# Kernel tuning notes

Measured on AMD Instinct MI355X. Metric: run time of the kernel, lower is better.

## Reference

```python
import jax, jax.numpy as jnp
import numpy as np

N = 100_000   # nodes
E = 1_600_000 # edges per edge type
DIN = 128     # input_dim
DH = 128      # prot_hidden_dim
L = 3         # prot_num_layers
EPS = 1e-5


def setup_inputs() -> dict:
    key = jax.random.key(0)
    ks = jax.random.split(key, 8)
    s = 1.0 / np.sqrt(DH)
    return {
        "x": jax.random.normal(ks[0], (N, DIN), jnp.float32),
        "src": jax.random.randint(ks[1], (3, E), 0, N, jnp.int32),
        "dst": jax.random.randint(ks[2], (3, E), 0, N, jnp.int32),
        "gc_W0": jax.random.normal(ks[3], (3, DIN, DH), jnp.float32) * s,
        "gc_b0": jnp.zeros((3, DH), jnp.float32),
        "gc_W": jax.random.normal(ks[4], (L - 1, 3, DH, DH), jnp.float32) * s,
        "gc_b": jnp.zeros((L - 1, 3, DH), jnp.float32),
        "fc_W": jax.random.normal(ks[5], (L, DH, DH), jnp.float32) * s,
        "fc_b": jnp.zeros((L, DH), jnp.float32),
        "bn_gamma": jnp.ones((L, DH), jnp.float32),
        "bn_beta": jnp.zeros((L, DH), jnp.float32),
    }


def _graph_conv(x, src, dst, W, b):
    # DGL GraphConv, norm='both': D_in^{-1/2} A D_out^{-1/2} X W + b
    ones = jnp.ones(src.shape[0], x.dtype)
    deg_out = jnp.clip(jax.ops.segment_sum(ones, src, num_segments=N), 1.0)
    deg_in = jnp.clip(jax.ops.segment_sum(ones, dst, num_segments=N), 1.0)
    # apply weight first (same math; keeps gathered message width = DH)
    h = (x * jax.lax.rsqrt(deg_out)[:, None]) @ W  # [N, DH]
    agg = jax.ops.segment_sum(h[src], dst, num_segments=N)  # gather + scatter-add
    return agg * jax.lax.rsqrt(deg_in)[:, None] + b


def _batchnorm(x, gamma, beta):
    # training-mode BatchNorm1d: biased batch statistics
    mu = jnp.mean(x, axis=0)
    var = jnp.mean(jnp.square(x - mu), axis=0)
    return (x - mu) * jax.lax.rsqrt(var + EPS) * gamma + beta


def reference(x, src, dst, gc_W0, gc_b0, gc_W, gc_b, fc_W, fc_b, bn_gamma, bn_beta):
    h = x
    for l in range(L):
        W = gc_W0 if l == 0 else gc_W[l - 1]
        b = gc_b0 if l == 0 else gc_b[l - 1]
        # HeteroGraphConv with aggregate='sum' over 3 edge types
        out = _graph_conv(h, src[0], dst[0], W[0], b[0])
        for e in range(1, 3):
            out = out + _graph_conv(h, src[e], dst[e], W[e], b[e])
        # FC -> ReLU -> BatchNorm (dropout = identity in eval mode)
        h = _batchnorm(jax.nn.relu(out @ fc_W[l] + fc_b[l]), bn_gamma[l], bn_beta[l])
    return h
```

## Files before the change

kernel.cpp:

```cpp
#include <hip/hip_runtime.h>


#define EPSV 1e-5f
#define CH 8192
#define MAXNB 512

typedef __attribute__((ext_vector_type(8))) short s8v;
typedef __attribute__((ext_vector_type(4))) float f4v;

__global__ void coarse_hist(const int* __restrict__ src, const int* __restrict__ dst,
                            int* __restrict__ chd, int* __restrict__ chs,
                            int E, int NB) {
    __shared__ int hd[MAXNB], hs[MAXNB];
    int t = blockIdx.y;
    for (int i = threadIdx.x; i < NB; i += 256) { hd[i] = 0; hs[i] = 0; }
    __syncthreads();
    int base = blockIdx.x * CH;
    int end = base + CH < E ? base + CH : E;
    const int* sp = src + (size_t)t * E;
    const int* dp = dst + (size_t)t * E;
    for (int i = base + threadIdx.x; i < end; i += 256) {
        atomicAdd(&hd[dp[i] >> 8], 1);
        atomicAdd(&hs[sp[i] >> 8], 1);
    }
    __syncthreads();
    for (int b = threadIdx.x; b < NB; b += 256) {
        if (hd[b]) atomicAdd(&chd[t * NB + b], hd[b]);
        if (hs[b]) atomicAdd(&chs[t * NB + b], hs[b]);
    }
}

__global__ void scan_off(const int* __restrict__ chd, const int* __restrict__ chs,
                         int* __restrict__ offd, int* __restrict__ offs,
                         int* __restrict__ gcd, int* __restrict__ gcs,
                         int* __restrict__ rowptr, int NB, int N, int E) {
    __shared__ int s[MAXNB];
    int tid = threadIdx.x;
    for (int a = 0; a < 6; ++a) {
        const int* h = (a < 3) ? chd + a * NB : chs + (a - 3) * NB;
        int* off = (a < 3) ? offd + a * (NB + 1) : offs + (a - 3) * (NB + 1);
        int* gc = (a < 3) ? gcd + a * NB : gcs + (a - 3) * NB;
        s[tid] = (tid < NB) ? h[tid] : 0;
        __syncthreads();
        for (int o = 1; o < MAXNB; o <<= 1) {
            int v = (tid >= o) ? s[tid - o] : 0;
            __syncthreads();
            s[tid] += v;
            __syncthreads();
        }
        if (tid < NB) {
            off[tid + 1] = s[tid];
            if (tid == 0) off[0] = 0;
        }
        __syncthreads();
        if (tid < NB) gc[tid] = off[tid];
        __syncthreads();
    }
    if (tid < 3) rowptr[tid * (N + 1) + N] = E;
}

__global__ void scatter_coarse(const int* __restrict__ src, const int* __restrict__ dst,
                               int* __restrict__ gcd, int* __restrict__ gcs,
                               int* __restrict__ dbuf, unsigned char* __restrict__ sbuf,
                               int E, int NB) {
    __shared__ int hd[MAXNB], hs[MAXNB], bd[MAXNB], bs[MAXNB];
    int t = blockIdx.y;
    for (int i = threadIdx.x; i < NB; i += 256) { hd[i] = 0; hs[i] = 0; }
    __syncthreads();
    int base = blockIdx.x * CH;
    int end = base + CH < E ? base + CH : E;
    const int* sp = src + (size_t)t * E;
    const int* dp = dst + (size_t)t * E;
    for (int i = base + threadIdx.x; i < end; i += 256) {
        atomicAdd(&hd[dp[i] >> 8], 1);
        atomicAdd(&hs[sp[i] >> 8], 1);
    }
    __syncthreads();
    for (int b = threadIdx.x; b < NB; b += 256) {
        bd[b] = hd[b] ? atomicAdd(&gcd[t * NB + b], hd[b]) : 0;
        bs[b] = hs[b] ? atomicAdd(&gcs[t * NB + b], hs[b]) : 0;
        hd[b] = 0;
        hs[b] = 0;
    }
    __syncthreads();
    for (int i = base + threadIdx.x; i < end; i += 256) {
        int sv = sp[i], dv = dp[i];
        int pb = dv >> 8;
        int pos = bd[pb] + atomicAdd(&hd[pb], 1);
        dbuf[(size_t)t * E + pos] = (sv << 8) | (dv & 255);
        int sb = sv >> 8;
        int ps = bs[sb] + atomicAdd(&hs[sb], 1);
        sbuf[(size_t)t * E + ps] = (unsigned char)(sv & 255);
    }
}

__global__ void fine_dst(const int* __restrict__ dbuf, const int* __restrict__ offd,
                         int* __restrict__ esrc, int* __restrict__ rowptr,
                         float* __restrict__ dri, int E, int N, int NB) {
    __shared__ int h[256], sc[256], cur[256];
    int b = blockIdx.x, t = blockIdx.y;
    int tid = threadIdx.x;
    h[tid] = 0;
    __syncthreads();
    int beg = offd[t * (NB + 1) + b], end = offd[t * (NB + 1) + b + 1];
    const int* dp = dbuf + (size_t)t * E;
    for (int i = beg + tid; i < end; i += 256) atomicAdd(&h[dp[i] & 255], 1);
    __syncthreads();
    sc[tid] = h[tid];
    __syncthreads();
    for (int o = 1; o < 256; o <<= 1) {
        int v = (tid >= o) ? sc[tid - o] : 0;
        __syncthreads();
        sc[tid] += v;
        __syncthreads();
    }
    int excl = sc[tid] - h[tid];
    cur[tid] = excl;
    int node = b * 256 + tid;
    if (node < N) {
        rowptr[t * (N + 1) + node] = beg + excl;
        int dg = h[tid] < 1 ? 1 : h[tid];
        dri[(size_t)t * N + node] = rsqrtf((float)dg);
    }
    __syncthreads();
    for (int i = beg + tid; i < end; i += 256) {
        int v = dp[i];
        int f = v & 255;
        int pos = beg + atomicAdd(&cur[f], 1);
        esrc[(size_t)t * E + pos] = v >> 8;
    }
}

__global__ void fine_src(const unsigned char* __restrict__ sbuf, const int* __restrict__ offs,
                         float* __restrict__ dro, int E, int N, int NB) {
    __shared__ int h[256];
    int b = blockIdx.x, t = blockIdx.y;
    int tid = threadIdx.x;
    h[tid] = 0;
    __syncthreads();
    int beg = offs[t * (NB + 1) + b], end = offs[t * (NB + 1) + b + 1];
    const unsigned char* sp = sbuf + (size_t)t * E;
    for (int i = beg + tid; i < end; i += 256) atomicAdd(&h[sp[i]], 1);
    __syncthreads();
    int node = b * 256 + tid;
    if (node < N) {
        int dg = h[tid] < 1 ? 1 : h[tid];
        dro[(size_t)t * N + node] = rsqrtf((float)dg);
    }
}

__device__ __forceinline__ unsigned int bfr(float f) {
    unsigned int u = __float_as_uint(f);
    return (u + 0x7FFFu + ((u >> 16) & 1u)) >> 16;
}
__device__ __forceinline__ unsigned int pack2(float lo, float hi) {
    return bfr(lo) | (bfr(hi) << 16);
}
__device__ __forceinline__ float blo(unsigned int u) { return __uint_as_float(u << 16); }
__device__ __forceinline__ float bhi(unsigned int u) { return __uint_as_float(u & 0xFFFF0000u); }

__global__ void cvt_bf16(const float* __restrict__ h, unsigned short* __restrict__ h2,
                         int total8) {
    int i = blockIdx.x * 256 + threadIdx.x;
    if (i >= total8) return;
    const float4* hp = (const float4*)h + (size_t)i * 2;
    float4 v0 = hp[0], v1 = hp[1];
    uint4 o;
    o.x = pack2(v0.x, v0.y);
    o.y = pack2(v0.z, v0.w);
    o.z = pack2(v1.x, v1.y);
    o.w = pack2(v1.z, v1.w);
    ((uint4*)h2)[i] = o;
}

__global__ void pack_w(const float* __restrict__ gcW0, const float* __restrict__ gcW,
                       const float* __restrict__ fcW, unsigned short* __restrict__ Wg,
                       unsigned short* __restrict__ Wf) {
    int mat = blockIdx.x;
    const float* srcp;
    unsigned short* dstp;
    if (mat < 9) {
        int l = mat / 3, e = mat % 3;
        srcp = (l == 0) ? gcW0 + (size_t)e * 16384
                        : gcW + ((size_t)(l - 1) * 3 + e) * 16384;
        dstp = Wg + (size_t)mat * 16384;
    } else {
        srcp = fcW + (size_t)(mat - 9) * 16384;
        dstp = Wf + (size_t)(mat - 9) * 16384;
    }
    for (int p = threadIdx.x; p < 16384; p += 256) {
        int j = p & 7;
        int ln = (p >> 3) & 63;
        int nt = (p >> 9) & 7;
        int ks = p >> 12;
        int k = ks * 32 + (ln >> 4) * 8 + j;
        int n = nt * 16 + (ln & 15);
        dstp[p] = (unsigned short)bfr(srcp[k * 128 + n]);
    }
}

__launch_bounds__(256)
__global__ void agg_kernel(const unsigned short* __restrict__ h2, const int* __restrict__ rowptr,
                           const int* __restrict__ esrc, const float* __restrict__ dro,
                           const float* __restrict__ dri, unsigned short* __restrict__ z, int N) {
    int idx = blockIdx.x * 256 + threadIdx.x;
    int node = idx >> 5;
    int l2 = idx & 31;
    if (node >= N) return;
    int beg = rowptr[node];
    int end = rowptr[node + 1];
    const uint2* hp = (const uint2*)h2 + l2;
    float4 acc = make_float4(0.f, 0.f, 0.f, 0.f);
    int j = beg;
    for (; j + 4 <= end; j += 4) {
        int s0 = esrc[j], s1 = esrc[j + 1], s2 = esrc[j + 2], s3 = esrc[j + 3];
        float w0 = dro[s0], w1 = dro[s1], w2 = dro[s2], w3 = dro[s3];
        uint2 u0 = hp[(size_t)s0 * 32];
        uint2 u1 = hp[(size_t)s1 * 32];
        uint2 u2 = hp[(size_t)s2 * 32];
        uint2 u3 = hp[(size_t)s3 * 32];
        acc.x += w0 * blo(u0.x) + w1 * blo(u1.x) + w2 * blo(u2.x) + w3 * blo(u3.x);
        acc.y += w0 * bhi(u0.x) + w1 * bhi(u1.x) + w2 * bhi(u2.x) + w3 * bhi(u3.x);
        acc.z += w0 * blo(u0.y) + w1 * blo(u1.y) + w2 * blo(u2.y) + w3 * blo(u3.y);
        acc.w += w0 * bhi(u0.y) + w1 * bhi(u1.y) + w2 * bhi(u2.y) + w3 * bhi(u3.y);
    }
    for (; j < end; ++j) {
        int s0 = esrc[j];
        float w0 = dro[s0];
        uint2 u0 = hp[(size_t)s0 * 32];
        acc.x += w0 * blo(u0.x);
        acc.y += w0 * bhi(u0.x);
        acc.z += w0 * blo(u0.y);
        acc.w += w0 * bhi(u0.y);
    }
    float scl = dri[node];
    uint2 o;
    o.x = pack2(acc.x * scl, acc.y * scl);
    o.y = pack2(acc.z * scl, acc.w * scl);
    *(uint2*)(z + (size_t)node * 128 + l2 * 4) = o;
}

__launch_bounds__(256)
__global__ void mfma_gc(const unsigned short* __restrict__ z0,
                        const unsigned short* __restrict__ z1,
                        const unsigned short* __restrict__ z2,
                        const unsigned short* __restrict__ Wp,
                        const float* __restrict__ b3,
                        unsigned short* __restrict__ C, int M) {
    const int tid = threadIdx.x;
    const int l = tid & 63;
    const int wv = tid >> 6;
    const int wm = wv >> 1, wn = wv & 1;
    const int m0 = blockIdx.x * 128;
    const int lr = l & 15;
    const int lk = (l >> 4) * 8;
    f4v acc[4][4];
#pragma unroll
    for (int i = 0; i < 4; ++i)
#pragma unroll
        for (int j = 0; j < 4; ++j) acc[i][j] = (f4v){0.f, 0.f, 0.f, 0.f};

    int rowb[4];
#pragma unroll
    for (int mt = 0; mt < 4; ++mt) {
        int r = m0 + wm * 64 + mt * 16 + lr;
        rowb[mt] = (r < M) ? r : (M - 1);
    }
#pragma unroll
    for (int e = 0; e < 3; ++e) {
        const unsigned short* zp = (e == 0) ? z0 : (e == 1) ? z1 : z2;
        const unsigned short* wp = Wp + (size_t)e * 16384;
#pragma unroll
        for (int ks = 0; ks < 4; ++ks) {
            s8v a[4], b[4];
#pragma unroll
            for (int mt = 0; mt < 4; ++mt)
                a[mt] = *(const s8v*)(zp + (size_t)rowb[mt] * 128 + ks * 32 + lk);
#pragma unroll
            for (int nt = 0; nt < 4; ++nt)
                b[nt] = *(const s8v*)(wp + ks * 4096 + (wn * 4 + nt) * 512 + l * 8);
#pragma unroll
            for (int mt = 0; mt < 4; ++mt)
#pragma unroll
                for (int nt = 0; nt < 4; ++nt)
                    acc[mt][nt] = __builtin_amdgcn_mfma_f32_16x16x32_bf16(
                        a[mt], b[nt], acc[mt][nt], 0, 0, 0);
        }
    }
    float bs[4];
    int col[4];
#pragma unroll
    for (int nt = 0; nt < 4; ++nt) {
        col[nt] = wn * 64 + nt * 16 + lr;
        bs[nt] = b3[col[nt]] + b3[128 + col[nt]] + b3[256 + col[nt]];
    }
#pragma unroll
    for (int mt = 0; mt < 4; ++mt) {
#pragma unroll
        for (int r = 0; r < 4; ++r) {
            int row = m0 + wm * 64 + mt * 16 + (l >> 4) * 4 + r;
            if (row < M) {
                unsigned short* cp = C + (size_t)row * 128;
#pragma unroll
                for (int nt = 0; nt < 4; ++nt)
                    cp[col[nt]] = (unsigned short)bfr(acc[mt][nt][r] + bs[nt]);
            }
        }
    }
}

template <int MODE>
__launch_bounds__(256)
__global__ void mfma_fc(const unsigned short* __restrict__ A,
                        const unsigned short* __restrict__ Wp,
                        const float* __restrict__ bias,
                        unsigned short* __restrict__ outb, float* __restrict__ outf,
                        float* __restrict__ bnsum, int M) {
    __shared__ float red[256];
    const int tid = threadIdx.x;
    const int l = tid & 63;
    const int wv = tid >> 6;
    const int wm = wv >> 1, wn = wv & 1;
    const int m0 = blockIdx.x * 128;
    const int lr = l & 15;
    const int lk = (l >> 4) * 8;
    f4v acc[4][4];
#pragma unroll
    for (int i = 0; i < 4; ++i)
#pragma unroll
        for (int j = 0; j < 4; ++j) acc[i][j] = (f4v){0.f, 0.f, 0.f, 0.f};

    int rowb[4];
#pragma unroll
    for (int mt = 0; mt < 4; ++mt) {
        int r = m0 + wm * 64 + mt * 16 + lr;
        rowb[mt] = (r < M) ? r : (M - 1);
    }
#pragma unroll
    for (int ks = 0; ks < 4; ++ks) {
        s8v a[4], b[4];
#pragma unroll
        for (int mt = 0; mt < 4; ++mt)
            a[mt] = *(const s8v*)(A + (size_t)rowb[mt] * 128 + ks * 32 + lk);
#pragma unroll
        for (int nt = 0; nt < 4; ++nt)
            b[nt] = *(const s8v*)(Wp + ks * 4096 + (wn * 4 + nt) * 512 + l * 8);
#pragma unroll
        for (int mt = 0; mt < 4; ++mt)
#pragma unroll
            for (int nt = 0; nt < 4; ++nt)
                acc[mt][nt] = __builtin_amdgcn_mfma_f32_16x16x32_bf16(
                    a[mt], b[nt], acc[mt][nt], 0, 0, 0);
    }

    float bv[4], cs[4] = {}, cq[4] = {};
    int col[4];
#pragma unroll
    for (int nt = 0; nt < 4; ++nt) {
        col[nt] = wn * 64 + nt * 16 + lr;
        bv[nt] = bias[col[nt]];
    }
#pragma unroll
    for (int mt = 0; mt < 4; ++mt) {
#pragma unroll
        for (int r = 0; r < 4; ++r) {
            int row = m0 + wm * 64 + mt * 16 + (l >> 4) * 4 + r;
            if (row < M) {
#pragma unroll
                for (int nt = 0; nt < 4; ++nt) {
                    float v = acc[mt][nt][r] + bv[nt];
                    v = v > 0.f ? v : 0.f;
                    cs[nt] += v;
                    cq[nt] += v * v;
                    if (MODE == 0)
                        outb[(size_t)row * 128 + col[nt]] = (unsigned short)bfr(v);
                    else
                        outf[(size_t)row * 128 + col[nt]] = v;
                }
            }
        }
    }
    red[tid] = 0.f;
    __syncthreads();
#pragma unroll
    for (int nt = 0; nt < 4; ++nt) {
        atomicAdd(&red[col[nt]], cs[nt]);
        atomicAdd(&red[128 + col[nt]], cq[nt]);
    }
    __syncthreads();
    if (tid < 128) {
        atomicAdd(&bnsum[tid], red[tid]);
        atomicAdd(&bnsum[128 + tid], red[128 + tid]);
    }
}

__global__ void bn_fin(const float* __restrict__ bnsum, const float* __restrict__ gamma,
                       const float* __restrict__ beta, float* __restrict__ ss, int N) {
    int c = threadIdx.x;
    if (c >= 128) return;
    float invn = 1.0f / (float)N;
    float mean = bnsum[c] * invn;
    float var = bnsum[128 + c] * invn - mean * mean;
    float inv = rsqrtf(var + EPSV);
    float sc = gamma[c] * inv;
    ss[c] = sc;
    ss[128 + c] = beta[c] - mean * sc;
}

__global__ void bn_affine_bf16(unsigned short* __restrict__ h2, const float* __restrict__ ss,
                               int total8) {
    int i = blockIdx.x * 256 + threadIdx.x;
    if (i >= total8) return;
    uint4 v = ((const uint4*)h2)[i];
    int cb = (i & 15) * 8;
    float4 a0 = *(const float4*)&ss[cb];
    float4 a1 = *(const float4*)&ss[cb + 4];
    float4 b0 = *(const float4*)&ss[128 + cb];
    float4 b1 = *(const float4*)&ss[128 + cb + 4];
    uint4 o;
    o.x = pack2(blo(v.x) * a0.x + b0.x, bhi(v.x) * a0.y + b0.y);
    o.y = pack2(blo(v.y) * a0.z + b0.z, bhi(v.y) * a0.w + b0.w);
    o.z = pack2(blo(v.z) * a1.x + b1.x, bhi(v.z) * a1.y + b1.y);
    o.w = pack2(blo(v.w) * a1.z + b1.z, bhi(v.w) * a1.w + b1.w);
    ((uint4*)h2)[i] = o;
}

__global__ void bn_apply(float* __restrict__ h, const float* __restrict__ ss, int total4) {
    int i = blockIdx.x * 256 + threadIdx.x;
    if (i >= total4) return;
    int c4 = (i & 31) * 4;
    float4 sc = *(const float4*)&ss[c4];
    float4 sh = *(const float4*)&ss[128 + c4];
    float4 v = ((float4*)h)[i];
    v.x = v.x * sc.x + sh.x;
    v.y = v.y * sc.y + sh.y;
    v.z = v.z * sc.z + sh.z;
    v.w = v.w * sc.w + sh.w;
    ((float4*)h)[i] = v;
}

extern "C" void kernel_launch(void* const* d_in, const int* in_sizes, int n_in,
                              void* d_out, int out_size, void* d_ws, size_t ws_size,
                              hipStream_t stream) {
    const float* x    = (const float*)d_in[0];
    const int*   src  = (const int*)d_in[1];
    const int*   dst  = (const int*)d_in[2];
    const float* gcW0 = (const float*)d_in[3];
    const float* gcb0 = (const float*)d_in[4];
    const float* gcW  = (const float*)d_in[5];
    const float* gcb  = (const float*)d_in[6];
    const float* fcW  = (const float*)d_in[7];
    const float* fcb  = (const float*)d_in[8];
    const float* bng  = (const float*)d_in[9];
    const float* bnb  = (const float*)d_in[10];
    float* out = (float*)d_out;

    const int N = in_sizes[0] / 128;
    const int E = in_sizes[1] / 3;
    const int NB = (N + 255) / 256;

    char* w = (char*)d_ws;
    auto alloc = [&](size_t bytes) -> char* {
        char* p = w;
        w += (bytes + 255) & ~(size_t)255;
        return p;
    };
    unsigned short* z0    = (unsigned short*)alloc((size_t)N * 128 * 2);
    unsigned short* z1    = (unsigned short*)alloc((size_t)N * 128 * 2);
    unsigned short* z2    = (unsigned short*)alloc((size_t)N * 128 * 2);
    unsigned short* gcout = (unsigned short*)alloc((size_t)N * 128 * 2);
    unsigned short* h2    = (unsigned short*)alloc((size_t)N * 128 * 2);
    unsigned short* Wg    = (unsigned short*)alloc((size_t)9 * 16384 * 2);
    unsigned short* Wf    = (unsigned short*)alloc((size_t)3 * 16384 * 2);
    int*   esrc   = (int*)alloc((size_t)3 * E * 4);
    int*   rowptr = (int*)alloc((size_t)3 * (N + 1) * 4);
    float* dro    = (float*)alloc((size_t)3 * N * 4);
    float* dri    = (float*)alloc((size_t)3 * N * 4);
    int*   chd    = (int*)alloc((size_t)3 * NB * 4);
    int*   chs    = (int*)alloc((size_t)3 * NB * 4);
    int*   offd   = (int*)alloc((size_t)3 * (NB + 1) * 4);
    int*   offs   = (int*)alloc((size_t)3 * (NB + 1) * 4);
    int*   gcd    = (int*)alloc((size_t)3 * NB * 4);
    int*   gcs    = (int*)alloc((size_t)3 * NB * 4);
    float* bnsum  = (float*)alloc(256 * 4);
    float* ss0    = (float*)alloc(256 * 4);
    float* ss1    = (float*)alloc(256 * 4);
    float* ss2    = (float*)alloc(256 * 4);
    int* dbuf = (int*)gcout;
    unsigned char* sbuf = (unsigned char*)z2;

    hipMemsetAsync(chd, 0, (size_t)3 * NB * 4, stream);
    hipMemsetAsync(chs, 0, (size_t)3 * NB * 4, stream);
    dim3 cg2((E + CH - 1) / CH, 3);
    coarse_hist<<<cg2, 256, 0, stream>>>(src, dst, chd, chs, E, NB);
    scan_off<<<1, MAXNB, 0, stream>>>(chd, chs, offd, offs, gcd, gcs, rowptr, NB, N, E);
    scatter_coarse<<<cg2, 256, 0, stream>>>(src, dst, gcd, gcs, dbuf, sbuf, E, NB);
    dim3 fg(NB, 3);
    fine_dst<<<fg, 256, 0, stream>>>(dbuf, offd, esrc, rowptr, dri, E, N, NB);
    fine_src<<<fg, 256, 0, stream>>>(sbuf, offs, dro, E, N, NB);

    pack_w<<<12, 256, 0, stream>>>(gcW0, gcW, fcW, Wg, Wf);
    const int cvtGrid = (N * 16 + 255) / 256;
    cvt_bf16<<<cvtGrid, 256, 0, stream>>>(x, h2, N * 16);

    const int gemmGrid = (N + 127) / 128;
    const int aggGrid = (N * 32 + 255) / 256;
    float* ssl[3] = {ss0, ss1, ss2};
    unsigned short* zb[3] = {z0, z1, z2};

    for (int l = 0; l < 3; ++l) {
        const float* bl = (l == 0) ? gcb0 : gcb + (size_t)(l - 1) * 3 * 128;
        for (int e = 0; e < 3; ++e)
            agg_kernel<<<aggGrid, 256, 0, stream>>>(h2, rowptr + e * (N + 1),
                                                    esrc + (size_t)e * E, dro + e * N,
                                                    dri + e * N, zb[e], N);
        mfma_gc<<<gemmGrid, 256, 0, stream>>>(z0, z1, z2, Wg + (size_t)l * 3 * 16384,
                                              bl, gcout, N);
        hipMemsetAsync(bnsum, 0, 256 * 4, stream);
        if (l < 2)
            mfma_fc<0><<<gemmGrid, 256, 0, stream>>>(gcout, Wf + (size_t)l * 16384,
                                                     fcb + (size_t)l * 128, h2, nullptr,
                                                     bnsum, N);
        else
            mfma_fc<1><<<gemmGrid, 256, 0, stream>>>(gcout, Wf + (size_t)l * 16384,
                                                     fcb + (size_t)l * 128, nullptr, out,
                                                     bnsum, N);
        bn_fin<<<1, 128, 0, stream>>>(bnsum, bng + (size_t)l * 128, bnb + (size_t)l * 128,
                                      ssl[l], N);
        if (l < 2)
            bn_affine_bf16<<<cvtGrid, 256, 0, stream>>>(h2, ssl[l], N * 16);
        else
            bn_apply<<<(N * 32 + 255) / 256, 256, 0, stream>>>(out, ssl[l], N * 32);
    }
}
```

Measured before the change: 1.076 ms.

## Stage scatter writes in LDS, widen aggregation loads, batch edge types, fuse BN finalize

The coarse scatter now sorts each chunk locally in shared memory and then writes contiguous runs to global memory, using a binary search to find each element's bucket. The fine dst pass also stages its output in LDS when the bucket fits. The aggregation kernel uses 16 lanes per node with 16-byte loads and an 8-way unrolled gather, and covers all three edge types in one launch via a 2D grid. BN finalize is folded into the affine kernels, which removes a launch per layer. The chunk size is halved to fit the LDS staging buffer, which means more blocks and more global atomics in the histogram passes.

```diff
diff --git a/kernel.cpp b/kernel.cpp
--- a/kernel.cpp
+++ b/kernel.cpp
@@ -2,7 +2,7 @@
 
 
 #define EPSV 1e-5f
-#define CH 8192
+#define CH 4096
 #define MAXNB 512
 
 typedef __attribute__((ext_vector_type(8))) short s8v;
@@ -13,7 +13,7 @@
                             int E, int NB) {
     __shared__ int hd[MAXNB], hs[MAXNB];
     int t = blockIdx.y;
-    for (int i = threadIdx.x; i < NB; i += 256) { hd[i] = 0; hs[i] = 0; }
+    for (int i = threadIdx.x; i < MAXNB; i += 256) { hd[i] = 0; hs[i] = 0; }
     __syncthreads();
     int base = blockIdx.x * CH;
     int end = base + CH < E ? base + CH : E;
@@ -59,50 +59,87 @@
     if (tid < 3) rowptr[tid * (N + 1) + N] = E;
 }
 
+__launch_bounds__(256)
 __global__ void scatter_coarse(const int* __restrict__ src, const int* __restrict__ dst,
                                int* __restrict__ gcd, int* __restrict__ gcs,
                                int* __restrict__ dbuf, unsigned char* __restrict__ sbuf,
                                int E, int NB) {
-    __shared__ int hd[MAXNB], hs[MAXNB], bd[MAXNB], bs[MAXNB];
-    int t = blockIdx.y;
-    for (int i = threadIdx.x; i < NB; i += 256) { hd[i] = 0; hs[i] = 0; }
-    __syncthreads();
-    int base = blockIdx.x * CH;
-    int end = base + CH < E ? base + CH : E;
+    __shared__ int hd[MAXNB], hs[MAXNB];
+    __shared__ int lod[MAXNB], los[MAXNB];
+    __shared__ int bd[MAXNB], bs[MAXNB];
+    __shared__ int rbi[CH];
+    __shared__ unsigned char rbs[CH];
+    const int tid = threadIdx.x;
+    const int t = blockIdx.y;
+    const int base = blockIdx.x * CH;
+    const int end = base + CH < E ? base + CH : E;
+    const int cnt = end - base;
     const int* sp = src + (size_t)t * E;
     const int* dp = dst + (size_t)t * E;
-    for (int i = base + threadIdx.x; i < end; i += 256) {
+
+    for (int i = tid; i < MAXNB; i += 256) { hd[i] = 0; hs[i] = 0; }
+    __syncthreads();
+    for (int i = base + tid; i < end; i += 256) {
         atomicAdd(&hd[dp[i] >> 8], 1);
         atomicAdd(&hs[sp[i] >> 8], 1);
     }
     __syncthreads();
-    for (int b = threadIdx.x; b < NB; b += 256) {
+    for (int b = tid; b < NB; b += 256) {
         bd[b] = hd[b] ? atomicAdd(&gcd[t * NB + b], hd[b]) : 0;
         bs[b] = hs[b] ? atomicAdd(&gcs[t * NB + b], hs[b]) : 0;
-        hd[b] = 0;
-        hs[b] = 0;
-    }
-    __syncthreads();
-    for (int i = base + threadIdx.x; i < end; i += 256) {
+    }
+    lod[tid] = hd[tid]; lod[tid + 256] = hd[tid + 256];
+    los[tid] = hs[tid]; los[tid + 256] = hs[tid + 256];
+    __syncthreads();
+    for (int o = 1; o < MAXNB; o <<= 1) {
+        int a0 = lod[tid], a1 = lod[tid + 256];
+        int b0 = los[tid], b1 = los[tid + 256];
+        int p0 = (tid >= o) ? lod[tid - o] : 0;
+        int p1 = lod[tid + 256 - o];
+        int q0 = (tid >= o) ? los[tid - o] : 0;
+        int q1 = los[tid + 256 - o];
+        __syncthreads();
+        lod[tid] = a0 + p0; lod[tid + 256] = a1 + p1;
+        los[tid] = b0 + q0; los[tid + 256] = b1 + q1;
+        __syncthreads();
+    }
+    hd[tid] = lod[tid] - hd[tid]; hd[tid + 256] = lod[tid + 256] - hd[tid + 256];
+    hs[tid] = los[tid] - hs[tid]; hs[tid + 256] = los[tid + 256] - hs[tid + 256];
+    __syncthreads();
+    for (int i = base + tid; i < end; i += 256) {
         int sv = sp[i], dv = dp[i];
-        int pb = dv >> 8;
-        int pos = bd[pb] + atomicAdd(&hd[pb], 1);
-        dbuf[(size_t)t * E + pos] = (sv << 8) | (dv & 255);
-        int sb = sv >> 8;
-        int ps = bs[sb] + atomicAdd(&hs[sb], 1);
-        sbuf[(size_t)t * E + ps] = (unsigned char)(sv & 255);
-    }
-}
-
+        int lp = atomicAdd(&hd[dv >> 8], 1);
+        rbi[lp] = (sv << 8) | (dv & 255);
+        int ls = atomicAdd(&hs[sv >> 8], 1);
+        rbs[ls] = (unsigned char)(sv & 255);
+    }
+    __syncthreads();
+    for (int i = tid; i < cnt; i += 256) {
+        int lo = 0, hi = NB - 1;
+        while (lo < hi) { int mid = (lo + hi) >> 1; if (lod[mid] > i) hi = mid; else lo = mid + 1; }
+        int excl = lo ? lod[lo - 1] : 0;
+        dbuf[(size_t)t * E + bd[lo] + (i - excl)] = rbi[i];
+    }
+    for (int i = tid; i < cnt; i += 256) {
+        int lo = 0, hi = NB - 1;
+        while (lo < hi) { int mid = (lo + hi) >> 1; if (los[mid] > i) hi = mid; else lo = mid + 1; }
+        int excl = lo ? los[lo - 1] : 0;
+        sbuf[(size_t)t * E + bs[lo] + (i - excl)] = rbs[i];
+    }
+}
+
+#define FDCAP 6656
 __global__ void fine_dst(const int* __restrict__ dbuf, const int* __restrict__ offd,
                          int* __restrict__ esrc, int* __restrict__ rowptr,
                          float* __restrict__ dri, int E, int N, int NB) {
     __shared__ int h[256], sc[256], cur[256];
+    __shared__ int rb[FDCAP];
     int b = blockIdx.x, t = blockIdx.y;
     int tid = threadIdx.x;
     h[tid] = 0;
     __syncthreads();
     int beg = offd[t * (NB + 1) + b], end = offd[t * (NB + 1) + b + 1];
+    int cnt = end - beg;
     const int* dp = dbuf + (size_t)t * E;
     for (int i = beg + tid; i < end; i += 256) atomicAdd(&h[dp[i] & 255], 1);
     __syncthreads();
@@ -123,11 +160,20 @@
         dri[(size_t)t * N + node] = rsqrtf((float)dg);
     }
     __syncthreads();
-    for (int i = beg + tid; i < end; i += 256) {
-        int v = dp[i];
-        int f = v & 255;
-        int pos = beg + atomicAdd(&cur[f], 1);
-        esrc[(size_t)t * E + pos] = v >> 8;
+    if (cnt <= FDCAP) {
+        for (int i = beg + tid; i < end; i += 256) {
+            int v = dp[i];
+            int p = atomicAdd(&cur[v & 255], 1);
+            rb[p] = v >> 8;
+        }
+        __syncthreads();
+        for (int i = tid; i < cnt; i += 256) esrc[(size_t)t * E + beg + i] = rb[i];
+    } else {
+        for (int i = beg + tid; i < end; i += 256) {
+            int v = dp[i];
+            int p = beg + atomicAdd(&cur[v & 255], 1);
+            esrc[(size_t)t * E + p] = v >> 8;
+        }
     }
 }
 
@@ -200,50 +246,81 @@
 }
 
 __launch_bounds__(256)
-__global__ void agg_kernel(const unsigned short* __restrict__ h2, const int* __restrict__ rowptr,
-                           const int* __restrict__ esrc, const float* __restrict__ dro,
-                           const float* __restrict__ dri, unsigned short* __restrict__ z, int N) {
+__global__ void agg_kernel(const unsigned short* __restrict__ h2, const int* __restrict__ rowptrB,
+                           const int* __restrict__ esrcB, const float* __restrict__ droB,
+                           const float* __restrict__ driB, unsigned short* __restrict__ zB,
+                           int N, int E) {
+    const int e = blockIdx.y;
+    const int* rowptr = rowptrB + e * (N + 1);
+    const int* esrc = esrcB + (size_t)e * E;
+    const float* dro = droB + (size_t)e * N;
+    const float* dri = driB + (size_t)e * N;
+    unsigned short* z = zB + (size_t)e * N * 128;
+
     int idx = blockIdx.x * 256 + threadIdx.x;
-    int node = idx >> 5;
-    int l2 = idx & 31;
+    int node = idx >> 4;
+    int lq = idx & 15;
     if (node >= N) return;
-    int beg = rowptr[node];
-    int end = rowptr[node + 1];
-    const uint2* hp = (const uint2*)h2 + l2;
-    float4 acc = make_float4(0.f, 0.f, 0.f, 0.f);
+    int beg = rowptr[node], end = rowptr[node + 1];
+    const uint4* hp = (const uint4*)h2 + lq;
+    float a0 = 0.f, a1 = 0.f, a2 = 0.f, a3 = 0.f, a4 = 0.f, a5 = 0.f, a6 = 0.f, a7 = 0.f;
     int j = beg;
+    for (; j + 8 <= end; j += 8) {
+        int s[8];
+#pragma unroll
+        for (int q = 0; q < 8; ++q) s[q] = esrc[j + q];
+        uint4 u[8];
+#pragma unroll
+        for (int q = 0; q < 8; ++q) u[q] = hp[(size_t)s[q] * 16];
+        float w[8];
+#pragma unroll
+        for (int q = 0; q < 8; ++q) w[q] = dro[s[q]];
+#pragma unroll
+        for (int q = 0; q < 8; ++q) {
+            a0 += w[q] * blo(u[q].x); a1 += w[q] * bhi(u[q].x);
+            a2 += w[q] * blo(u[q].y); a3 += w[q] * bhi(u[q].y);
+            a4 += w[q] * blo(u[q].z); a5 += w[q] * bhi(u[q].z);
+            a6 += w[q] * blo(u[q].w); a7 += w[q] * bhi(u[q].w);
+        }
+    }
     for (; j + 4 <= end; j += 4) {
-        int s0 = esrc[j], s1 = esrc[j + 1], s2 = esrc[j + 2], s3 = esrc[j + 3];
-        float w0 = dro[s0], w1 = dro[s1], w2 = dro[s2], w3 = dro[s3];
-        uint2 u0 = hp[(size_t)s0 * 32];
-        uint2 u1 = hp[(size_t)s1 * 32];
-        uint2 u2 = hp[(size_t)s2 * 32];
-        uint2 u3 = hp[(size_t)s3 * 32];
-        acc.x += w0 * blo(u0.x) + w1 * blo(u1.x) + w2 * blo(u2.x) + w3 * blo(u3.x);
-        acc.y += w0 * bhi(u0.x) + w1 * bhi(u1.x) + w2 * bhi(u2.x) + w3 * bhi(u3.x);
-        acc.z += w0 * blo(u0.y) + w1 * blo(u1.y) + w2 * blo(u2.y) + w3 * blo(u3.y);
-        acc.w += w0 * bhi(u0.y) + w1 * bhi(u1.y) + w2 * bhi(u2.y) + w3 * bhi(u3.y);
+        int s[4];
+#pragma unroll
+        for (int q = 0; q < 4; ++q) s[q] = esrc[j + q];
+        uint4 u[4];
+#pragma unroll
+        for (int q = 0; q < 4; ++q) u[q] = hp[(size_t)s[q] * 16];
+        float w[4];
+#pragma unroll
+        for (int q = 0; q < 4; ++q) w[q] = dro[s[q]];
+#pragma unroll
+        for (int q = 0; q < 4; ++q) {
+            a0 += w[q] * blo(u[q].x); a1 += w[q] * bhi(u[q].x);
+            a2 += w[q] * blo(u[q].y); a3 += w[q] * bhi(u[q].y);
+            a4 += w[q] * blo(u[q].z); a5 += w[q] * bhi(u[q].z);
+            a6 += w[q] * blo(u[q].w); a7 += w[q] * bhi(u[q].w);
+        }
     }
     for (; j < end; ++j) {
         int s0 = esrc[j];
         float w0 = dro[s0];
-        uint2 u0 = hp[(size_t)s0 * 32];
-        acc.x += w0 * blo(u0.x);
-        acc.y += w0 * bhi(u0.x);
-        acc.z += w0 * blo(u0.y);
-        acc.w += w0 * bhi(u0.y);
+        uint4 u0 = hp[(size_t)s0 * 16];
+        a0 += w0 * blo(u0.x); a1 += w0 * bhi(u0.x);
+        a2 += w0 * blo(u0.y); a3 += w0 * bhi(u0.y);
+        a4 += w0 * blo(u0.z); a5 += w0 * bhi(u0.z);
+        a6 += w0 * blo(u0.w); a7 += w0 * bhi(u0.w);
     }
     float scl = dri[node];
-    uint2 o;
-    o.x = pack2(acc.x * scl, acc.y * scl);
-    o.y = pack2(acc.z * scl, acc.w * scl);
-    *(uint2*)(z + (size_t)node * 128 + l2 * 4) = o;
+    uint4 o;
+    o.x = pack2(a0 * scl, a1 * scl);
+    o.y = pack2(a2 * scl, a3 * scl);
+    o.z = pack2(a4 * scl, a5 * scl);
+    o.w = pack2(a6 * scl, a7 * scl);
+    ((uint4*)z)[(size_t)node * 16 + lq] = o;
 }
 
 __launch_bounds__(256)
-__global__ void mfma_gc(const unsigned short* __restrict__ z0,
-                        const unsigned short* __restrict__ z1,
-                        const unsigned short* __restrict__ z2,
+__global__ void mfma_gc(const unsigned short* __restrict__ zB,
                         const unsigned short* __restrict__ Wp,
                         const float* __restrict__ b3,
                         unsigned short* __restrict__ C, int M) {
@@ -268,7 +345,7 @@
     }
 #pragma unroll
     for (int e = 0; e < 3; ++e) {
-        const unsigned short* zp = (e == 0) ? z0 : (e == 1) ? z1 : z2;
+        const unsigned short* zp = zB + (size_t)e * M * 128;
         const unsigned short* wp = Wp + (size_t)e * 16384;
 #pragma unroll
         for (int ks = 0; ks < 4; ++ks) {
@@ -394,29 +471,27 @@
     }
 }
 
-__global__ void bn_fin(const float* __restrict__ bnsum, const float* __restrict__ gamma,
-                       const float* __restrict__ beta, float* __restrict__ ss, int N) {
-    int c = threadIdx.x;
-    if (c >= 128) return;
-    float invn = 1.0f / (float)N;
-    float mean = bnsum[c] * invn;
-    float var = bnsum[128 + c] * invn - mean * mean;
-    float inv = rsqrtf(var + EPSV);
-    float sc = gamma[c] * inv;
-    ss[c] = sc;
-    ss[128 + c] = beta[c] - mean * sc;
-}
-
-__global__ void bn_affine_bf16(unsigned short* __restrict__ h2, const float* __restrict__ ss,
-                               int total8) {
-    int i = blockIdx.x * 256 + threadIdx.x;
+__global__ void bn_affine_bf16(unsigned short* __restrict__ h2, const float* __restrict__ bnsum,
+                               const float* __restrict__ gamma, const float* __restrict__ beta,
+                               float invn, int total8) {
+    __shared__ float lss[256];
+    int tid = threadIdx.x;
+    if (tid < 128) {
+        float mean = bnsum[tid] * invn;
+        float var = bnsum[128 + tid] * invn - mean * mean;
+        float sc = gamma[tid] * rsqrtf(var + EPSV);
+        lss[tid] = sc;
+        lss[128 + tid] = beta[tid] - mean * sc;
+    }
+    __syncthreads();
+    int i = blockIdx.x * 256 + tid;
     if (i >= total8) return;
     uint4 v = ((const uint4*)h2)[i];
     int cb = (i & 15) * 8;
-    float4 a0 = *(const float4*)&ss[cb];
-    float4 a1 = *(const float4*)&ss[cb + 4];
-    float4 b0 = *(const float4*)&ss[128 + cb];
-    float4 b1 = *(const float4*)&ss[128 + cb + 4];
+    float4 a0 = *(const float4*)&lss[cb];
+    float4 a1 = *(const float4*)&lss[cb + 4];
+    float4 b0 = *(const float4*)&lss[128 + cb];
+    float4 b1 = *(const float4*)&lss[128 + cb + 4];
     uint4 o;
     o.x = pack2(blo(v.x) * a0.x + b0.x, bhi(v.x) * a0.y + b0.y);
     o.y = pack2(blo(v.y) * a0.z + b0.z, bhi(v.y) * a0.w + b0.w);
@@ -425,12 +500,24 @@
     ((uint4*)h2)[i] = o;
 }
 
-__global__ void bn_apply(float* __restrict__ h, const float* __restrict__ ss, int total4) {
-    int i = blockIdx.x * 256 + threadIdx.x;
+__global__ void bn_apply(float* __restrict__ h, const float* __restrict__ bnsum,
+                         const float* __restrict__ gamma, const float* __restrict__ beta,
+                         float invn, int total4) {
+    __shared__ float lss[256];
+    int tid = threadIdx.x;
+    if (tid < 128) {
+        float mean = bnsum[tid] * invn;
+        float var = bnsum[128 + tid] * invn - mean * mean;
+        float sc = gamma[tid] * rsqrtf(var + EPSV);
+        lss[tid] = sc;
+        lss[128 + tid] = beta[tid] - mean * sc;
+    }
+    __syncthreads();
+    int i = blockIdx.x * 256 + tid;
     if (i >= total4) return;
     int c4 = (i & 31) * 4;
-    float4 sc = *(const float4*)&ss[c4];
-    float4 sh = *(const float4*)&ss[128 + c4];
+    float4 sc = *(const float4*)&lss[c4];
+    float4 sh = *(const float4*)&lss[128 + c4];
     float4 v = ((float4*)h)[i];
     v.x = v.x * sc.x + sh.x;
     v.y = v.y * sc.y + sh.y;
@@ -465,9 +552,7 @@
         w += (bytes + 255) & ~(size_t)255;
         return p;
     };
-    unsigned short* z0    = (unsigned short*)alloc((size_t)N * 128 * 2);
-    unsigned short* z1    = (unsigned short*)alloc((size_t)N * 128 * 2);
-    unsigned short* z2    = (unsigned short*)alloc((size_t)N * 128 * 2);
+    unsigned short* zB    = (unsigned short*)alloc((size_t)3 * N * 128 * 2);
     unsigned short* gcout = (unsigned short*)alloc((size_t)N * 128 * 2);
     unsigned short* h2    = (unsigned short*)alloc((size_t)N * 128 * 2);
     unsigned short* Wg    = (unsigned short*)alloc((size_t)9 * 16384 * 2);
@@ -483,11 +568,8 @@
     int*   gcd    = (int*)alloc((size_t)3 * NB * 4);
     int*   gcs    = (int*)alloc((size_t)3 * NB * 4);
     float* bnsum  = (float*)alloc(256 * 4);
-    float* ss0    = (float*)alloc(256 * 4);
-    float* ss1    = (float*)alloc(256 * 4);
-    float* ss2    = (float*)alloc(256 * 4);
-    int* dbuf = (int*)gcout;
-    unsigned char* sbuf = (unsigned char*)z2;
+    int* dbuf = (int*)zB;
+    unsigned char* sbuf = (unsigned char*)gcout;
 
     hipMemsetAsync(chd, 0, (size_t)3 * NB * 4, stream);
     hipMemsetAsync(chs, 0, (size_t)3 * NB * 4, stream);
@@ -504,18 +586,13 @@
     cvt_bf16<<<cvtGrid, 256, 0, stream>>>(x, h2, N * 16);
 
     const int gemmGrid = (N + 127) / 128;
-    const int aggGrid = (N * 32 + 255) / 256;
-    float* ssl[3] = {ss0, ss1, ss2};
-    unsigned short* zb[3] = {z0, z1, z2};
+    const float invn = 1.0f / (float)N;
+    dim3 aggG((N * 16 + 255) / 256, 3);
 
     for (int l = 0; l < 3; ++l) {
         const float* bl = (l == 0) ? gcb0 : gcb + (size_t)(l - 1) * 3 * 128;
-        for (int e = 0; e < 3; ++e)
-            agg_kernel<<<aggGrid, 256, 0, stream>>>(h2, rowptr + e * (N + 1),
-                                                    esrc + (size_t)e * E, dro + e * N,
-                                                    dri + e * N, zb[e], N);
-        mfma_gc<<<gemmGrid, 256, 0, stream>>>(z0, z1, z2, Wg + (size_t)l * 3 * 16384,
-                                              bl, gcout, N);
+        agg_kernel<<<aggG, 256, 0, stream>>>(h2, rowptr, esrc, dro, dri, zB, N, E);
+        mfma_gc<<<gemmGrid, 256, 0, stream>>>(zB, Wg + (size_t)l * 3 * 16384, bl, gcout, N);
         hipMemsetAsync(bnsum, 0, 256 * 4, stream);
         if (l < 2)
             mfma_fc<0><<<gemmGrid, 256, 0, stream>>>(gcout, Wf + (size_t)l * 16384,
@@ -525,11 +602,13 @@
             mfma_fc<1><<<gemmGrid, 256, 0, stream>>>(gcout, Wf + (size_t)l * 16384,
                                                      fcb + (size_t)l * 128, nullptr, out,
                                                      bnsum, N);
-        bn_fin<<<1, 128, 0, stream>>>(bnsum, bng + (size_t)l * 128, bnb + (size_t)l * 128,
-                                      ssl[l], N);
         if (l < 2)
-            bn_affine_bf16<<<cvtGrid, 256, 0, stream>>>(h2, ssl[l], N * 16);
+            bn_affine_bf16<<<cvtGrid, 256, 0, stream>>>(h2, bnsum, bng + (size_t)l * 128,
+                                                        bnb + (size_t)l * 128, invn, N * 16);
         else
-            bn_apply<<<(N * 32 + 255) / 256, 256, 0, stream>>>(out, ssl[l], N * 32);
-    }
-}
+            bn_apply<<<(N * 32 + 255) / 256, 256, 0, stream>>>(out, bnsum,
+                                                               bng + (size_t)l * 128,
+                                                               bnb + (size_t)l * 128, invn,
+                                                               N * 32);
+    }
+}
```

Result: faster. 997.3 us (-7.3%).
